# Performance work log

Hardware: AMD Instinct MI355X
Metric: run time of the kernel (lower is better)

The kernel has to match this reference:

```python
import jax, jax.numpy as jnp
import numpy as np

D_MODEL = 1024
D_STATE = 16
D_CONV = 4
EXPAND = 2
D_INNER = EXPAND * D_MODEL          # 2048
DT_RANK = (D_MODEL + 15) // 16      # 64 (mamba 'auto')
B, L = 2, 1024


def _mamba_params(key, scale=0.02):
    ks = jax.random.split(key, 6)
    return dict(
        inW=jax.random.normal(ks[0], (2 * D_INNER, D_MODEL), jnp.float32) * scale,
        convW=jax.random.normal(ks[1], (D_INNER, 1, D_CONV), jnp.float32) * scale,
        convb=jnp.zeros((D_INNER,), jnp.float32),
        xprojW=jax.random.normal(ks[2], (DT_RANK + 2 * D_STATE, D_INNER), jnp.float32) * scale,
        dtW=jax.random.normal(ks[3], (D_INNER, DT_RANK), jnp.float32) * scale,
        dtb=jax.random.normal(ks[4], (D_INNER,), jnp.float32) * scale,
        A_log=jnp.log(jnp.tile(jnp.arange(1, D_STATE + 1, dtype=jnp.float32), (D_INNER, 1))),
        Dskip=jnp.ones((D_INNER,), jnp.float32),
        outW=jax.random.normal(ks[5], (D_MODEL, D_INNER), jnp.float32) * scale,
    )


def setup_inputs() -> dict:
    key = jax.random.key(0)
    kx, kf, kb, kp = jax.random.split(key, 4)
    inp = {"x": jax.random.normal(kx, (B, L, D_MODEL), jnp.float32)}
    inp["ln_w"] = jnp.ones((D_MODEL,), jnp.float32)
    inp["ln_b"] = jnp.zeros((D_MODEL,), jnp.float32)
    for pref, k in (("f_", kf), ("b_", kb)):
        for name, v in _mamba_params(k).items():
            inp[pref + name] = v
    inp["proj_W"] = jax.random.normal(kp, (D_MODEL, 2 * D_MODEL), jnp.float32) * 0.02
    inp["proj_b"] = jnp.zeros((D_MODEL,), jnp.float32)
    return inp


def _layernorm(x, w, b, eps=1e-5):
    mu = jnp.mean(x, axis=-1, keepdims=True)
    var = jnp.var(x, axis=-1, keepdims=True)
    return (x - mu) * jax.lax.rsqrt(var + eps) * w + b


def _mamba(x, inW, convW, convb, xprojW, dtW, dtb, A_log, Dskip, outW):
    # x: [B, L, d_model]
    xz = jnp.einsum('bld,ed->ble', x, inW)           # [B,L,2*d_inner]
    xs, z = jnp.split(xz, 2, axis=-1)                # each [B,L,d_inner]
    # depthwise causal conv over L
    xc = jnp.transpose(xs, (0, 2, 1))                # [B,d_inner,L]
    xc = jax.lax.conv_general_dilated(
        xc, convW, window_strides=(1,), padding=[(D_CONV - 1, 0)],
        feature_group_count=D_INNER)
    xs = jax.nn.silu(jnp.transpose(xc + convb[None, :, None], (0, 2, 1)))
    # input-dependent dt, B, C
    xdb = jnp.einsum('bld,ed->ble', xs, xprojW)      # [B,L,dt_rank+2*d_state]
    dt, Bm, Cm = jnp.split(xdb, [DT_RANK, DT_RANK + D_STATE], axis=-1)
    dt = jax.nn.softplus(jnp.einsum('blr,dr->bld', dt, dtW) + dtb)  # [B,L,d_inner]
    A = -jnp.exp(A_log)                              # [d_inner,d_state], negative
    dA = jnp.exp(dt[..., None] * A)                  # [B,L,d_inner,d_state]
    dBx = dt[..., None] * Bm[:, :, None, :] * xs[..., None]

    def step(h, inputs):
        dA_t, dBx_t, C_t = inputs                    # [B,d,s],[B,d,s],[B,s]
        h = h * dA_t + dBx_t
        y = jnp.einsum('bds,bs->bd', h, C_t)
        return h, y

    h0 = jnp.zeros((x.shape[0], D_INNER, D_STATE), x.dtype)
    _, ys = jax.lax.scan(step, h0, (jnp.moveaxis(dA, 1, 0),
                                    jnp.moveaxis(dBx, 1, 0),
                                    jnp.moveaxis(Cm, 1, 0)))
    y = jnp.moveaxis(ys, 0, 1)                       # [B,L,d_inner]
    y = (y + xs * Dskip) * jax.nn.silu(z)
    return jnp.einsum('bld,ed->ble', y, outW)        # [B,L,d_model]


def reference(x, ln_w, ln_b,
              f_inW, f_convW, f_convb, f_xprojW, f_dtW, f_dtb, f_A_log, f_Dskip, f_outW,
              b_inW, b_convW, b_convb, b_xprojW, b_dtW, b_dtb, b_A_log, b_Dskip, b_outW,
              proj_W, proj_b):
    normed = _layernorm(x, ln_w, ln_b)
    fwd_out = _mamba(normed, f_inW, f_convW, f_convb, f_xprojW, f_dtW, f_dtb,
                     f_A_log, f_Dskip, f_outW)
    bwd_out = _mamba(normed[:, ::-1, :], b_inW, b_convW, b_convb, b_xprojW, b_dtW,
                     b_dtb, b_A_log, b_Dskip, b_outW)[:, ::-1, :]
    combined = jnp.concatenate([fwd_out, bwd_out], axis=-1)
    return x + jnp.einsum('blc,ec->ble', combined, proj_W) + proj_b
```

## Files before the change

kernel.cpp:

```cpp
#include <hip/hip_runtime.h>
#include <hip/hip_bf16.h>
#include <math.h>

#define DM   1024
#define DI   2048
#define DTR  64
#define DST  16
#define NB   2
#define LL   1024
#define MR   (NB*LL)
#define XLD  128
#define KS   8

typedef __bf16 bf16x8 __attribute__((ext_vector_type(8)));
typedef float  f32x4  __attribute__((ext_vector_type(4)));

__device__ __forceinline__ float siluf(float x) { return x / (1.f + __expf(-x)); }
__device__ __forceinline__ float softplusf(float x) {
    return fmaxf(x, 0.f) + log1pf(__expf(-fabsf(x)));
}
__device__ __forceinline__ unsigned short f2bf(float f) {
    __hip_bfloat16 h = __float2bfloat16(f);
    return *reinterpret_cast<unsigned short*>(&h);
}
__device__ __forceinline__ float bf2f(__hip_bfloat16 h) { return __bfloat162float(h); }

__device__ __forceinline__ void gl2lds16(const __hip_bfloat16* g, __hip_bfloat16* l)
{
    __builtin_amdgcn_global_load_lds(
        (const __attribute__((address_space(1))) unsigned int*)g,
        (__attribute__((address_space(3))) unsigned int*)l, 16, 0, 0);
}

__global__ __launch_bounds__(256) void layernorm_k(
    const float* __restrict__ x, const float* __restrict__ w,
    const float* __restrict__ b, __hip_bfloat16* __restrict__ out)
{
    int row = blockIdx.x;
    int tid = threadIdx.x;
    const float* xr = x + (size_t)row * DM;
    float4 v = *(const float4*)(xr + tid * 4);
    float s = v.x + v.y + v.z + v.w;
    float q = v.x*v.x + v.y*v.y + v.z*v.z + v.w*v.w;
    #pragma unroll
    for (int off = 32; off > 0; off >>= 1) {
        s += __shfl_xor(s, off, 64);
        q += __shfl_xor(q, off, 64);
    }
    __shared__ float ss[4], qq[4];
    int wv = tid >> 6;
    if ((tid & 63) == 0) { ss[wv] = s; qq[wv] = q; }
    __syncthreads();
    s = ss[0] + ss[1] + ss[2] + ss[3];
    q = qq[0] + qq[1] + qq[2] + qq[3];
    float mu  = s * (1.f / DM);
    float var = q * (1.f / DM) - mu * mu;
    float rstd = rsqrtf(var + 1e-5f);
    float4 wv4 = *(const float4*)(w + tid * 4);
    float4 bv4 = *(const float4*)(b + tid * 4);
    ushort4 o;
    o.x = f2bf((v.x - mu) * rstd * wv4.x + bv4.x);
    o.y = f2bf((v.y - mu) * rstd * wv4.y + bv4.y);
    o.z = f2bf((v.z - mu) * rstd * wv4.z + bv4.z);
    o.w = f2bf((v.w - mu) * rstd * wv4.w + bv4.w);
    *(ushort4*)((unsigned short*)out + (size_t)row * DM + tid * 4) = o;
}

__global__ __launch_bounds__(256) void cvt_all_k(
    const float* __restrict__ s0, const float* __restrict__ s1,
    const float* __restrict__ s2, const float* __restrict__ s3,
    const float* __restrict__ s4, __hip_bfloat16* __restrict__ dst)
{
    long idx = (long)(blockIdx.x * 256 + threadIdx.x) * 4;
    const float* src; long off;
    if      (idx <  4194304L) { src = s0; off = idx; }
    else if (idx <  8388608L) { src = s1; off = idx -  4194304L; }
    else if (idx < 10485760L) { src = s2; off = idx -  8388608L; }
    else if (idx < 10616832L) { src = s3; off = idx - 10485760L; }
    else                      { src = s4; off = idx - 10616832L; }
    float4 v = *(const float4*)(src + off);
    ushort4 o;
    o.x = f2bf(v.x); o.y = f2bf(v.y); o.z = f2bf(v.z); o.w = f2bf(v.w);
    *(ushort4*)((unsigned short*)dst + idx) = o;
}

__global__ __launch_bounds__(256) void cvt_pad96_k(
    const float* __restrict__ f_in, const float* __restrict__ b_in,
    __hip_bfloat16* __restrict__ out)
{
    int z = blockIdx.y;
    const float* in = z ? b_in : f_in;
    int idx = (blockIdx.x * 256 + threadIdx.x) * 4;
    int row = idx >> 11;
    ushort4 o = make_ushort4(0, 0, 0, 0);
    if (row < 96) {
        float4 v = *(const float4*)(in + idx);
        o.x = f2bf(v.x); o.y = f2bf(v.y); o.z = f2bf(v.z); o.w = f2bf(v.w);
    }
    *(ushort4*)((unsigned short*)out + (size_t)z * 128 * DI + idx) = o;
}

__global__ __launch_bounds__(256) void transpose_k(
    const float* __restrict__ f_o, const float* __restrict__ b_o,
    __hip_bfloat16* __restrict__ wot)
{
    int z = blockIdx.z;
    const float* src = z ? b_o : f_o;
    int c0 = blockIdx.x * 64;
    int r0 = blockIdx.y * 64;
    __shared__ float t[64][65];
    int tc = threadIdx.x & 63;
    int tr = threadIdx.x >> 6;
    #pragma unroll
    for (int ii = 0; ii < 16; ++ii) {
        int rl = tr + ii * 4;
        t[tc][rl] = src[(size_t)(r0 + rl) * DI + c0 + tc];
    }
    __syncthreads();
    __hip_bfloat16* dst = wot + (size_t)z * DI * DM;
    #pragma unroll
    for (int ii = 0; ii < 16; ++ii) {
        int cl = tr + ii * 4;
        dst[(size_t)(c0 + cl) * DM + r0 + tc] = __float2bfloat16(t[cl][tc]);
    }
}

template<int EPI>
__global__ __launch_bounds__(256) void gemm_gl(
    const __hip_bfloat16* __restrict__ A, int lda, size_t aofs,
    const __hip_bfloat16* __restrict__ B, int ldb, size_t bofs,
    void* __restrict__ Cp, int ldc, size_t cofs, int K,
    const float* __restrict__ bias0, const float* __restrict__ bias1)
{
    __shared__ __hip_bfloat16 As[128 * 64];
    __shared__ __hip_bfloat16 Bs[128 * 64];
    const int tid  = threadIdx.x;
    const int z    = blockIdx.z;
    const int bm   = blockIdx.y * 128;
    const int bn   = blockIdx.x * 128;
    const __hip_bfloat16* Az = A + (size_t)z * aofs;
    const __hip_bfloat16* Bz = B + (size_t)z * bofs;
    const int wv   = tid >> 6;
    const int lane = tid & 63;
    const int wr   = (wv >> 1) * 64;
    const int wc   = (wv & 1) * 64;
    const int srow = wv * 32 + (lane >> 3);
    const int cg   = ((lane & 7) ^ (lane >> 3)) * 8;
    const int fr   = lane & 15;
    const int quad = lane >> 4;
    const int pc0  = (quad ^ (fr & 7)) * 8;
    const int pc1  = ((4 + quad) ^ (fr & 7)) * 8;

    f32x4 acc[4][4] = {};

    for (int k0 = 0; k0 < K; k0 += 64) {
        __syncthreads();
        #pragma unroll
        for (int i = 0; i < 4; ++i) {
            int r = srow + i * 8;
            gl2lds16(Az + (size_t)(bm + r) * lda + k0 + cg, As + wv * 2048 + i * 512);
            gl2lds16(Bz + (size_t)(bn + r) * ldb + k0 + cg, Bs + wv * 2048 + i * 512);
        }
        __syncthreads();
        #pragma unroll
        for (int kk = 0; kk < 2; ++kk) {
            const int pc = kk ? pc1 : pc0;
            bf16x8 af[4], bf_[4];
            #pragma unroll
            for (int i = 0; i < 4; ++i) {
                af[i]  = *(const bf16x8*)(As + (wr + i * 16 + fr) * 64 + pc);
                bf_[i] = *(const bf16x8*)(Bs + (wc + i * 16 + fr) * 64 + pc);
            }
            #pragma unroll
            for (int i = 0; i < 4; ++i)
                #pragma unroll
                for (int j = 0; j < 4; ++j)
                    acc[i][j] = __builtin_amdgcn_mfma_f32_16x16x32_bf16(
                        af[i], bf_[j], acc[i][j], 0, 0, 0);
        }
    }

    const float* bias = (EPI == 3) ? (z ? bias1 : bias0) : nullptr;
    const int er = quad * 4;
    const int ec = fr;
    #pragma unroll
    for (int i = 0; i < 4; ++i) {
        #pragma unroll
        for (int j = 0; j < 4; ++j) {
            int row = bm + wr + i * 16 + er;
            int col = bn + wc + j * 16 + ec;
            #pragma unroll
            for (int r = 0; r < 4; ++r) {
                float v = acc[i][j][r];
                if (EPI == 1) {
                    ((__hip_bfloat16*)Cp)[(size_t)z * cofs +
                        (size_t)(row + r) * ldc + col] = __float2bfloat16(v);
                } else if (EPI == 3) {
                    ((__hip_bfloat16*)Cp)[(size_t)z * cofs +
                        (size_t)(row + r) * ldc + col] =
                        __float2bfloat16(softplusf(v + bias[col]));
                } else {
                    ((float*)Cp)[(size_t)z * cofs + (size_t)(row + r) * ldc + col] = v;
                }
            }
        }
    }
}

__global__ __launch_bounds__(256) void xproj_part_k(
    const __hip_bfloat16* __restrict__ A,
    const __hip_bfloat16* __restrict__ B,
    float* __restrict__ part)
{
    __shared__ __hip_bfloat16 As[128 * 64];
    __shared__ __hip_bfloat16 Bs[128 * 64];
    const int tid  = threadIdx.x;
    const int ks   = blockIdx.x;
    const int bm   = blockIdx.y * 128;
    const int z    = blockIdx.z;
    const __hip_bfloat16* Az = A + (size_t)z * MR * DI;
    const __hip_bfloat16* Bz = B + (size_t)z * 128 * DI;
    const int kb   = ks * (DI / KS);
    const int wv   = tid >> 6;
    const int lane = tid & 63;
    const int wr   = (wv >> 1) * 64;
    const int wc   = (wv & 1) * 64;
    const int srow = wv * 32 + (lane >> 3);
    const int cg   = ((lane & 7) ^ (lane >> 3)) * 8;
    const int fr   = lane & 15;
    const int quad = lane >> 4;
    const int pc0  = (quad ^ (fr & 7)) * 8;
    const int pc1  = ((4 + quad) ^ (fr & 7)) * 8;

    f32x4 acc[4][4] = {};

    #pragma unroll
    for (int k0 = 0; k0 < DI / KS; k0 += 64) {
        __syncthreads();
        #pragma unroll
        for (int i = 0; i < 4; ++i) {
            int r = srow + i * 8;
            gl2lds16(Az + (size_t)(bm + r) * DI + kb + k0 + cg, As + wv * 2048 + i * 512);
            gl2lds16(Bz + (size_t)r * DI + kb + k0 + cg,        Bs + wv * 2048 + i * 512);
        }
        __syncthreads();
        #pragma unroll
        for (int kk = 0; kk < 2; ++kk) {
            const int pc = kk ? pc1 : pc0;
            bf16x8 af[4], bf_[4];
            #pragma unroll
            for (int i = 0; i < 4; ++i) {
                af[i]  = *(const bf16x8*)(As + (wr + i * 16 + fr) * 64 + pc);
                bf_[i] = *(const bf16x8*)(Bs + (wc + i * 16 + fr) * 64 + pc);
            }
            #pragma unroll
            for (int i = 0; i < 4; ++i)
                #pragma unroll
                for (int j = 0; j < 4; ++j)
                    acc[i][j] = __builtin_amdgcn_mfma_f32_16x16x32_bf16(
                        af[i], bf_[j], acc[i][j], 0, 0, 0);
        }
    }

    float* dst = part + ((size_t)z * KS + ks) * MR * XLD;
    const int er = quad * 4;
    const int ec = fr;
    #pragma unroll
    for (int i = 0; i < 4; ++i)
        #pragma unroll
        for (int j = 0; j < 4; ++j) {
            int row = bm + wr + i * 16 + er;
            int col = wc + j * 16 + ec;
            #pragma unroll
            for (int r = 0; r < 4; ++r)
                dst[(size_t)(row + r) * XLD + col] = acc[i][j][r];
        }
}

__global__ __launch_bounds__(256) void xproj_reduce_k(
    const float* __restrict__ part, float* __restrict__ xdb,
    __hip_bfloat16* __restrict__ xdbt)
{
    int z = blockIdx.y;
    size_t idx = ((size_t)blockIdx.x * 256 + threadIdx.x) * 4;
    const float* p = part + (size_t)z * KS * MR * XLD;
    float4 s = make_float4(0.f, 0.f, 0.f, 0.f);
    #pragma unroll
    for (int ks = 0; ks < KS; ++ks) {
        float4 v = *(const float4*)(p + (size_t)ks * MR * XLD + idx);
        s.x += v.x; s.y += v.y; s.z += v.z; s.w += v.w;
    }
    *(float4*)(xdb + (size_t)z * MR * XLD + idx) = s;
    int c = (int)(idx & (XLD - 1));
    if (c < 64) {
        size_t m = idx >> 7;
        ushort4 o;
        o.x = f2bf(s.x); o.y = f2bf(s.y); o.z = f2bf(s.z); o.w = f2bf(s.w);
        *(ushort4*)((unsigned short*)xdbt + (size_t)z * MR * 64 + m * 64 + c) = o;
    }
}

__global__ __launch_bounds__(256) void conv_silu_k(
    const __hip_bfloat16* __restrict__ xz2,
    const float* __restrict__ fW, const float* __restrict__ fb,
    const float* __restrict__ bW, const float* __restrict__ bb_,
    __hip_bfloat16* __restrict__ xsb2)
{
    int dirv = blockIdx.y;
    int idx = blockIdx.x * 256 + threadIdx.x;
    int d = idx & (DI - 1);
    int m = idx >> 11;
    int t = m & (LL - 1);
    int bb = m >> 10;
    const float* w  = (dirv ? bW : fW) + d * 4;
    const __hip_bfloat16* xz = xz2 + (size_t)dirv * MR * 2 * DI;
    float acc = (dirv ? bb_ : fb)[d];
    if (dirv == 0) {
        #pragma unroll
        for (int k = 0; k < 4; ++k) {
            int tt = t - 3 + k;
            if (tt >= 0)
                acc = fmaf(w[k], bf2f(xz[(size_t)(bb * LL + tt) * (2 * DI) + d]), acc);
        }
    } else {
        #pragma unroll
        for (int k = 0; k < 4; ++k) {
            int tt = t + 3 - k;
            if (tt < LL)
                acc = fmaf(w[k], bf2f(xz[(size_t)(bb * LL + tt) * (2 * DI) + d]), acc);
        }
    }
    xsb2[(size_t)dirv * MR * DI + (size_t)m * DI + d] = __float2bfloat16(siluf(acc));
}

__global__ __launch_bounds__(256) void scan1_k(
    const __hip_bfloat16* __restrict__ dtf2, const __hip_bfloat16* __restrict__ xsb2,
    const float* __restrict__ xdb2,
    const float* __restrict__ fA, const float* __restrict__ bA,
    float* __restrict__ hend, float* __restrict__ aprod, int G, int Cn)
{
    int d  = blockIdx.x * 256 + threadIdx.x;
    int bb = blockIdx.y;
    int zz = blockIdx.z;
    int dirv = (zz >= G) ? 1 : 0;
    int g = zz - (dirv ? G : 0);
    const float* A_log = dirv ? bA : fA;
    const __hip_bfloat16* dtf = dtf2 + (size_t)dirv * MR * DI;
    const __hip_bfloat16* xs = xsb2 + (size_t)dirv * MR * DI;
    const float* xdb = xdb2 + (size_t)dirv * MR * XLD;
    size_t hoff = (size_t)dirv * G * (NB * DI * DST);

    float Ad[DST], h[DST], ap[DST];
    bool pw = true;
    #pragma unroll
    for (int s = 0; s < DST; ++s) {
        Ad[s] = -__expf(A_log[d * DST + s]);
        pw = pw && (fabsf(Ad[s] + (float)(s + 1)) < 1e-3f * (s + 1));
        h[s] = 0.f; ap[s] = 1.f;
    }
    int i0 = g * Cn;
    for (int i = 0; i < Cn; ++i) {
        int ii = i0 + i;
        int t = dirv ? (LL - 1 - ii) : ii;
        size_t m = (size_t)bb * LL + t;
        float dtv = bf2f(dtf[m * DI + d]);
        float xv  = bf2f(xs[m * DI + d]);
        const float* bc = xdb + m * XLD;
        float dtx = dtv * xv;
        float dAv[DST];
        if (pw) {
            float r = __expf(-dtv);
            float a = r;
            #pragma unroll
            for (int s = 0; s < DST; ++s) { dAv[s] = a; a *= r; }
        } else {
            #pragma unroll
            for (int s = 0; s < DST; ++s) dAv[s] = __expf(dtv * Ad[s]);
        }
        #pragma unroll
        for (int s = 0; s < DST; ++s) {
            h[s] = fmaf(h[s], dAv[s], dtx * bc[64 + s]);
            ap[s] *= dAv[s];
        }
    }
    size_t base = hoff + ((size_t)(g * NB + bb) * DI + d) * DST;
    #pragma unroll
    for (int s = 0; s < DST; s += 4) {
        *(float4*)(hend  + base + s) = make_float4(h[s], h[s+1], h[s+2], h[s+3]);
        *(float4*)(aprod + base + s) = make_float4(ap[s], ap[s+1], ap[s+2], ap[s+3]);
    }
}

__global__ __launch_bounds__(256) void scan2_k(
    float* __restrict__ hend, const float* __restrict__ aprod, int G)
{
    int dirv = blockIdx.y;
    int idx = blockIdx.x * 256 + threadIdx.x;
    const int slab = NB * DI * DST;
    size_t hoff = (size_t)dirv * G * slab;
    float carry = 0.f;
    for (int g = 0; g < G; ++g) {
        size_t off = hoff + (size_t)g * slab + idx;
        float a = aprod[off];
        float e = hend[off];
        hend[off] = carry;
        carry = fmaf(a, carry, e);
    }
}

__global__ __launch_bounds__(256) void scan3_k(
    const __hip_bfloat16* __restrict__ dtf2, const __hip_bfloat16* __restrict__ xsb2,
    const float* __restrict__ xdb2, const __hip_bfloat16* __restrict__ xz2,
    const float* __restrict__ fA, const float* __restrict__ bA,
    const float* __restrict__ fD, const float* __restrict__ bD,
    const float* __restrict__ hin, __hip_bfloat16* __restrict__ ycat, int G, int Cn)
{
    int d  = blockIdx.x * 256 + threadIdx.x;
    int bb = blockIdx.y;
    int zz = blockIdx.z;
    int dirv = (zz >= G) ? 1 : 0;
    int g = zz - (dirv ? G : 0);
    const float* A_log = dirv ? bA : fA;
    const float* Dskip = dirv ? bD : fD;
    const __hip_bfloat16* dtf = dtf2 + (size_t)dirv * MR * DI;
    const __hip_bfloat16* xs = xsb2 + (size_t)dirv * MR * DI;
    const float* xdb = xdb2 + (size_t)dirv * MR * XLD;
    const __hip_bfloat16* xz = xz2 + (size_t)dirv * MR * 2 * DI;
    size_t hoff = (size_t)dirv * G * (NB * DI * DST);

    float Ad[DST], h[DST];
    bool pw = true;
    size_t base = hoff + ((size_t)(g * NB + bb) * DI + d) * DST;
    #pragma unroll
    for (int s = 0; s < DST; ++s) {
        Ad[s] = -__expf(A_log[d * DST + s]);
        pw = pw && (fabsf(Ad[s] + (float)(s + 1)) < 1e-3f * (s + 1));
        h[s] = hin[base + s];
    }
    float Dsk = Dskip[d];
    int i0 = g * Cn;
    for (int i = 0; i < Cn; ++i) {
        int ii = i0 + i;
        int t = dirv ? (LL - 1 - ii) : ii;
        size_t m = (size_t)bb * LL + t;
        float dtv = bf2f(dtf[m * DI + d]);
        float xv  = bf2f(xs[m * DI + d]);
        const float* bc = xdb + m * XLD;
        float dtx = dtv * xv;
        float dAv[DST];
        if (pw) {
            float r = __expf(-dtv);
            float a = r;
            #pragma unroll
            for (int s = 0; s < DST; ++s) { dAv[s] = a; a *= r; }
        } else {
            #pragma unroll
            for (int s = 0; s < DST; ++s) dAv[s] = __expf(dtv * Ad[s]);
        }
        float yv = 0.f;
        #pragma unroll
        for (int s = 0; s < DST; ++s) {
            h[s] = fmaf(h[s], dAv[s], dtx * bc[64 + s]);
            yv = fmaf(h[s], bc[80 + s], yv);
        }
        float zv = bf2f(xz[m * (2 * DI) + DI + d]);
        ycat[m * (2 * DI) + (size_t)dirv * DI + d] =
            __float2bfloat16((yv + xv * Dsk) * siluf(zv));
    }
}

__global__ __launch_bounds__(256) void scan_mono_k(
    const __hip_bfloat16* __restrict__ dtf2, const __hip_bfloat16* __restrict__ xsb2,
    const float* __restrict__ xdb2, const __hip_bfloat16* __restrict__ xz2,
    const float* __restrict__ fA, const float* __restrict__ bA,
    const float* __restrict__ fD, const float* __restrict__ bD,
    __hip_bfloat16* __restrict__ ycat)
{
    int d  = blockIdx.x * 256 + threadIdx.x;
    int bb = blockIdx.y;
    int dirv = blockIdx.z;
    const float* A_log = dirv ? bA : fA;
    const float* Dskip = dirv ? bD : fD;
    const __hip_bfloat16* dtf = dtf2 + (size_t)dirv * MR * DI;
    const __hip_bfloat16* xs = xsb2 + (size_t)dirv * MR * DI;
    const float* xdb = xdb2 + (size_t)dirv * MR * XLD;
    const __hip_bfloat16* xz = xz2 + (size_t)dirv * MR * 2 * DI;
    float Ad[DST], h[DST];
    #pragma unroll
    for (int s = 0; s < DST; ++s) { Ad[s] = -__expf(A_log[d * DST + s]); h[s] = 0.f; }
    float Dsk = Dskip[d];
    for (int i = 0; i < LL; ++i) {
        int t = dirv ? (LL - 1 - i) : i;
        size_t m = (size_t)bb * LL + t;
        float dtv = bf2f(dtf[m * DI + d]);
        float xv  = bf2f(xs[m * DI + d]);
        const float* bc = xdb + m * XLD;
        float dtx = dtv * xv;
        float yv = 0.f;
        #pragma unroll
        for (int s = 0; s < DST; ++s) {
            float dA = __expf(dtv * Ad[s]);
            h[s] = fmaf(h[s], dA, dtx * bc[64 + s]);
            yv = fmaf(h[s], bc[80 + s], yv);
        }
        float zv = bf2f(xz[m * (2 * DI) + DI + d]);
        ycat[m * (2 * DI) + (size_t)dirv * DI + d] =
            __float2bfloat16((yv + xv * Dsk) * siluf(zv));
    }
}

__global__ __launch_bounds__(256) void final_reduce_k(
    const float* __restrict__ part, const float* __restrict__ x,
    const float* __restrict__ proj_b, float* __restrict__ out)
{
    size_t idx = ((size_t)blockIdx.x * 256 + threadIdx.x) * 4;
    float4 s = make_float4(0.f, 0.f, 0.f, 0.f);
    #pragma unroll
    for (int z = 0; z < 4; ++z) {
        float4 v = *(const float4*)(part + (size_t)z * MR * DM + idx);
        s.x += v.x; s.y += v.y; s.z += v.z; s.w += v.w;
    }
    float4 xv = *(const float4*)(x + idx);
    int col = (int)(idx & (DM - 1));
    float4 pb = *(const float4*)(proj_b + col);
    float4 o;
    o.x = xv.x + pb.x + s.x;
    o.y = xv.y + pb.y + s.y;
    o.z = xv.z + pb.z + s.z;
    o.w = xv.w + pb.w + s.w;
    *(float4*)(out + idx) = o;
}

extern "C" void kernel_launch(void* const* d_in, const int* in_sizes, int n_in,
                              void* d_out, int out_size, void* d_ws, size_t ws_size,
                              hipStream_t stream)
{
    const float* x      = (const float*)d_in[0];
    const float* ln_w   = (const float*)d_in[1];
    const float* ln_b   = (const float*)d_in[2];
    const float* f_inW    = (const float*)d_in[3];
    const float* f_convW  = (const float*)d_in[4];
    const float* f_convb  = (const float*)d_in[5];
    const float* f_xprojW = (const float*)d_in[6];
    const float* f_dtW    = (const float*)d_in[7];
    const float* f_dtb    = (const float*)d_in[8];
    const float* f_A_log  = (const float*)d_in[9];
    const float* f_Dskip  = (const float*)d_in[10];
    const float* f_outW   = (const float*)d_in[11];
    const float* b_inW    = (const float*)d_in[12];
    const float* b_convW  = (const float*)d_in[13];
    const float* b_convb  = (const float*)d_in[14];
    const float* b_xprojW = (const float*)d_in[15];
    const float* b_dtW    = (const float*)d_in[16];
    const float* b_dtb    = (const float*)d_in[17];
    const float* b_A_log  = (const float*)d_in[18];
    const float* b_Dskip  = (const float*)d_in[19];
    const float* b_outW   = (const float*)d_in[20];
    const float* proj_W = (const float*)d_in[21];
    const float* proj_b = (const float*)d_in[22];

    float* ws = (float*)d_ws;
    size_t o = 0;
    __hip_bfloat16* xz2  = (__hip_bfloat16*)(ws + o);
    __hip_bfloat16* wot  = xz2;
    float* fpart = ws + o;
    o += (size_t)2 * MR * 2 * DI / 2;
    __hip_bfloat16* xsb2 = (__hip_bfloat16*)(ws + o); o += (size_t)2 * MR * DI / 2;
    __hip_bfloat16* ycat = (__hip_bfloat16*)(ws + o);
    float* xpart = ws + o;
    o += (size_t)MR * 2 * DI / 2;
    float* xdb2 = ws + o; o += (size_t)2 * MR * XLD;
    __hip_bfloat16* xdbt = (__hip_bfloat16*)(ws + o); o += (size_t)2 * MR * 64 / 2;
    __hip_bfloat16* dtfb = (__hip_bfloat16*)(ws + o); o += (size_t)2 * MR * DI / 2;
    __hip_bfloat16* nb = (__hip_bfloat16*)(ws + o); o += (size_t)MR * DM / 2;
    __hip_bfloat16* warena = (__hip_bfloat16*)(ws + o); o += 15466496 / 2;
    float* hbuf = ws + o;
    size_t base_floats = o;

    __hip_bfloat16* wbi  = warena;
    __hip_bfloat16* pwb  = warena +  8388608;
    __hip_bfloat16* wdt  = warena + 10485760;
    __hip_bfloat16* wpb2 = warena + 10747904;
    __hip_bfloat16* wcat = warena + 11272192;

    const size_t slab = (size_t)NB * DI * DST;
    int G = 32;
    while (G > 4 && (base_floats + 4ull * G * slab) * 4 > ws_size) G >>= 1;
    int useChunks = ((base_floats + 4ull * G * slab) * 4 <= ws_size);
    float* hend  = hbuf;
    float* aprod = hbuf + 2ull * G * slab;
    int Cn = useChunks ? LL / G : LL;

    cvt_all_k<<<10496, 256, 0, stream>>>(f_inW, b_inW, proj_W, f_dtW, b_dtW, warena);
    cvt_pad96_k<<<dim3(64, 2), 256, 0, stream>>>(f_xprojW, b_xprojW, wpb2);
    transpose_k<<<dim3(DI / 64, DM / 64, 2), 256, 0, stream>>>(f_outW, b_outW, wot);
    gemm_gl<1><<<dim3(DI / 128, DM / 128, 2), 256, 0, stream>>>(
        pwb, 2 * DM, (size_t)DM, wot, DM, (size_t)DI * DM,
        wcat, 2 * DI, (size_t)DI, DM, nullptr, nullptr);

    layernorm_k<<<MR, 256, 0, stream>>>(x, ln_w, ln_b, nb);

    gemm_gl<1><<<dim3((2 * DI) / 128, MR / 128, 2), 256, 0, stream>>>(
        nb, DM, 0, wbi, DM, (size_t)2 * DI * DM,
        xz2, 2 * DI, (size_t)MR * 2 * DI, DM, nullptr, nullptr);

    conv_silu_k<<<dim3((MR * DI) / 256, 2), 256, 0, stream>>>(
        xz2, f_convW, f_convb, b_convW, b_convb, xsb2);

    xproj_part_k<<<dim3(KS, MR / 128, 2), 256, 0, stream>>>(xsb2, wpb2, xpart);
    xproj_reduce_k<<<dim3((MR * XLD) / 1024, 2), 256, 0, stream>>>(xpart, xdb2, xdbt);

    gemm_gl<3><<<dim3(DI / 128, MR / 128, 2), 256, 0, stream>>>(
        xdbt, 64, (size_t)MR * 64, wdt, 64, (size_t)DI * 64,
        dtfb, DI, (size_t)MR * DI, 64, f_dtb, b_dtb);

    if (useChunks) {
        scan1_k<<<dim3(DI / 256, NB, 2 * G), 256, 0, stream>>>(
            dtfb, xsb2, xdb2, f_A_log, b_A_log, hend, aprod, G, Cn);
        scan2_k<<<dim3((NB * DI * DST) / 256, 2), 256, 0, stream>>>(hend, aprod, G);
        scan3_k<<<dim3(DI / 256, NB, 2 * G), 256, 0, stream>>>(
            dtfb, xsb2, xdb2, xz2, f_A_log, b_A_log, f_Dskip, b_Dskip,
            hend, ycat, G, Cn);
    } else {
        scan_mono_k<<<dim3(DI / 256, NB, 2), 256, 0, stream>>>(
            dtfb, xsb2, xdb2, xz2, f_A_log, b_A_log, f_Dskip, b_Dskip, ycat);
    }

    gemm_gl<0><<<dim3(DM / 128, MR / 128, 4), 256, 0, stream>>>(
        ycat, 2 * DI, 1024, wcat, 2 * DI, 1024,
        fpart, DM, (size_t)MR * DM, 1024, nullptr, nullptr);

    final_reduce_k<<<(MR * DM) / 1024, 256, 0, stream>>>(
        fpart, x, proj_b, (float*)d_out);
}
```

Before: 424.8 us.

## Fuse prep kernels, use atomic split-K output, and coalesce GEMM epilogue via LDS

Result: no change. 431.2 us (+1.5%).

```diff
diff --git a/kernel.cpp b/kernel.cpp
--- a/kernel.cpp
+++ b/kernel.cpp
@@ -32,96 +32,100 @@
         (__attribute__((address_space(3))) unsigned int*)l, 16, 0, 0);
 }
 
-__global__ __launch_bounds__(256) void layernorm_k(
-    const float* __restrict__ x, const float* __restrict__ w,
-    const float* __restrict__ b, __hip_bfloat16* __restrict__ out)
-{
-    int row = blockIdx.x;
-    int tid = threadIdx.x;
-    const float* xr = x + (size_t)row * DM;
-    float4 v = *(const float4*)(xr + tid * 4);
-    float s = v.x + v.y + v.z + v.w;
-    float q = v.x*v.x + v.y*v.y + v.z*v.z + v.w*v.w;
-    #pragma unroll
-    for (int off = 32; off > 0; off >>= 1) {
-        s += __shfl_xor(s, off, 64);
-        q += __shfl_xor(q, off, 64);
-    }
-    __shared__ float ss[4], qq[4];
-    int wv = tid >> 6;
-    if ((tid & 63) == 0) { ss[wv] = s; qq[wv] = q; }
-    __syncthreads();
-    s = ss[0] + ss[1] + ss[2] + ss[3];
-    q = qq[0] + qq[1] + qq[2] + qq[3];
-    float mu  = s * (1.f / DM);
-    float var = q * (1.f / DM) - mu * mu;
-    float rstd = rsqrtf(var + 1e-5f);
-    float4 wv4 = *(const float4*)(w + tid * 4);
-    float4 bv4 = *(const float4*)(b + tid * 4);
-    ushort4 o;
-    o.x = f2bf((v.x - mu) * rstd * wv4.x + bv4.x);
-    o.y = f2bf((v.y - mu) * rstd * wv4.y + bv4.y);
-    o.z = f2bf((v.z - mu) * rstd * wv4.z + bv4.z);
-    o.w = f2bf((v.w - mu) * rstd * wv4.w + bv4.w);
-    *(ushort4*)((unsigned short*)out + (size_t)row * DM + tid * 4) = o;
-}
-
-__global__ __launch_bounds__(256) void cvt_all_k(
+__global__ __launch_bounds__(256) void prep_k(
     const float* __restrict__ s0, const float* __restrict__ s1,
     const float* __restrict__ s2, const float* __restrict__ s3,
-    const float* __restrict__ s4, __hip_bfloat16* __restrict__ dst)
-{
-    long idx = (long)(blockIdx.x * 256 + threadIdx.x) * 4;
-    const float* src; long off;
-    if      (idx <  4194304L) { src = s0; off = idx; }
-    else if (idx <  8388608L) { src = s1; off = idx -  4194304L; }
-    else if (idx < 10485760L) { src = s2; off = idx -  8388608L; }
-    else if (idx < 10616832L) { src = s3; off = idx - 10485760L; }
-    else                      { src = s4; off = idx - 10616832L; }
-    float4 v = *(const float4*)(src + off);
-    ushort4 o;
-    o.x = f2bf(v.x); o.y = f2bf(v.y); o.z = f2bf(v.z); o.w = f2bf(v.w);
-    *(ushort4*)((unsigned short*)dst + idx) = o;
-}
-
-__global__ __launch_bounds__(256) void cvt_pad96_k(
-    const float* __restrict__ f_in, const float* __restrict__ b_in,
-    __hip_bfloat16* __restrict__ out)
-{
-    int z = blockIdx.y;
-    const float* in = z ? b_in : f_in;
-    int idx = (blockIdx.x * 256 + threadIdx.x) * 4;
-    int row = idx >> 11;
-    ushort4 o = make_ushort4(0, 0, 0, 0);
-    if (row < 96) {
-        float4 v = *(const float4*)(in + idx);
+    const float* __restrict__ s4, __hip_bfloat16* __restrict__ warena,
+    const float* __restrict__ fx, const float* __restrict__ bx,
+    __hip_bfloat16* __restrict__ wpb2,
+    const float* __restrict__ fo, const float* __restrict__ bo,
+    __hip_bfloat16* __restrict__ wot,
+    const float* __restrict__ x, const float* __restrict__ lnw,
+    const float* __restrict__ lnb, __hip_bfloat16* __restrict__ nb,
+    const float* __restrict__ proj_b, float* __restrict__ outp)
+{
+    __shared__ float pshm[64 * 65];
+    const int b = blockIdx.x;
+    const int tid = threadIdx.x;
+
+    if (b < 10496) {
+        long idx = (long)b * 1024 + tid * 4;
+        const float* src; long off;
+        if      (idx <  4194304L) { src = s0; off = idx; }
+        else if (idx <  8388608L) { src = s1; off = idx -  4194304L; }
+        else if (idx < 10485760L) { src = s2; off = idx -  8388608L; }
+        else if (idx < 10616832L) { src = s3; off = idx - 10485760L; }
+        else                      { src = s4; off = idx - 10616832L; }
+        float4 v = *(const float4*)(src + off);
+        ushort4 o;
         o.x = f2bf(v.x); o.y = f2bf(v.y); o.z = f2bf(v.z); o.w = f2bf(v.w);
-    }
-    *(ushort4*)((unsigned short*)out + (size_t)z * 128 * DI + idx) = o;
-}
-
-__global__ __launch_bounds__(256) void transpose_k(
-    const float* __restrict__ f_o, const float* __restrict__ b_o,
-    __hip_bfloat16* __restrict__ wot)
-{
-    int z = blockIdx.z;
-    const float* src = z ? b_o : f_o;
-    int c0 = blockIdx.x * 64;
-    int r0 = blockIdx.y * 64;
-    __shared__ float t[64][65];
-    int tc = threadIdx.x & 63;
-    int tr = threadIdx.x >> 6;
-    #pragma unroll
-    for (int ii = 0; ii < 16; ++ii) {
-        int rl = tr + ii * 4;
-        t[tc][rl] = src[(size_t)(r0 + rl) * DI + c0 + tc];
-    }
-    __syncthreads();
-    __hip_bfloat16* dst = wot + (size_t)z * DI * DM;
-    #pragma unroll
-    for (int ii = 0; ii < 16; ++ii) {
-        int cl = tr + ii * 4;
-        dst[(size_t)(c0 + cl) * DM + r0 + tc] = __float2bfloat16(t[cl][tc]);
+        *(ushort4*)((unsigned short*)warena + idx) = o;
+    } else if (b < 10624) {
+        int t = b - 10496;
+        int z = t >> 6;
+        const float* in = z ? bx : fx;
+        int idx = ((t & 63) * 256 + tid) * 4;
+        int row = idx >> 11;
+        ushort4 o = make_ushort4(0, 0, 0, 0);
+        if (row < 96) {
+            float4 v = *(const float4*)(in + idx);
+            o.x = f2bf(v.x); o.y = f2bf(v.y); o.z = f2bf(v.z); o.w = f2bf(v.w);
+        }
+        *(ushort4*)((unsigned short*)wpb2 + (size_t)z * 128 * DI + idx) = o;
+    } else if (b < 11648) {
+        int t = b - 10624;
+        int z = t >> 9; t &= 511;
+        const float* src = z ? bo : fo;
+        int c0 = (t & 31) * 64;
+        int r0 = (t >> 5) * 64;
+        int tc = tid & 63;
+        int tr = tid >> 6;
+        #pragma unroll
+        for (int ii = 0; ii < 16; ++ii) {
+            int rl = tr + ii * 4;
+            pshm[tc * 65 + rl] = src[(size_t)(r0 + rl) * DI + c0 + tc];
+        }
+        __syncthreads();
+        __hip_bfloat16* dst = wot + (size_t)z * DI * DM;
+        #pragma unroll
+        for (int ii = 0; ii < 16; ++ii) {
+            int cl = tr + ii * 4;
+            dst[(size_t)(c0 + cl) * DM + r0 + tc] = __float2bfloat16(pshm[cl * 65 + tc]);
+        }
+    } else if (b < 13696) {
+        int row = b - 11648;
+        const float* xr = x + (size_t)row * DM;
+        float4 v = *(const float4*)(xr + tid * 4);
+        float s = v.x + v.y + v.z + v.w;
+        float q = v.x*v.x + v.y*v.y + v.z*v.z + v.w*v.w;
+        #pragma unroll
+        for (int off = 32; off > 0; off >>= 1) {
+            s += __shfl_xor(s, off, 64);
+            q += __shfl_xor(q, off, 64);
+        }
+        int wv = tid >> 6;
+        if ((tid & 63) == 0) { pshm[wv] = s; pshm[8 + wv] = q; }
+        __syncthreads();
+        s = pshm[0] + pshm[1] + pshm[2] + pshm[3];
+        q = pshm[8] + pshm[9] + pshm[10] + pshm[11];
+        float mu  = s * (1.f / DM);
+        float var = q * (1.f / DM) - mu * mu;
+        float rstd = rsqrtf(var + 1e-5f);
+        float4 wv4 = *(const float4*)(lnw + tid * 4);
+        float4 bv4 = *(const float4*)(lnb + tid * 4);
+        ushort4 o;
+        o.x = f2bf((v.x - mu) * rstd * wv4.x + bv4.x);
+        o.y = f2bf((v.y - mu) * rstd * wv4.y + bv4.y);
+        o.z = f2bf((v.z - mu) * rstd * wv4.z + bv4.z);
+        o.w = f2bf((v.w - mu) * rstd * wv4.w + bv4.w);
+        *(ushort4*)((unsigned short*)nb + (size_t)row * DM + tid * 4) = o;
+    } else {
+        size_t idx = ((size_t)(b - 13696) * 256 + tid) * 4;
+        float4 xv = *(const float4*)(x + idx);
+        float4 pb = *(const float4*)(proj_b + (idx & (DM - 1)));
+        float4 o;
+        o.x = xv.x + pb.x; o.y = xv.y + pb.y; o.z = xv.z + pb.z; o.w = xv.w + pb.w;
+        *(float4*)(outp + idx) = o;
     }
 }
 
@@ -132,8 +136,9 @@
     void* __restrict__ Cp, int ldc, size_t cofs, int K,
     const float* __restrict__ bias0, const float* __restrict__ bias1)
 {
-    __shared__ __hip_bfloat16 As[128 * 64];
-    __shared__ __hip_bfloat16 Bs[128 * 64];
+    __shared__ __hip_bfloat16 smem[2 * 128 * 64];
+    __hip_bfloat16* As = smem;
+    __hip_bfloat16* Bs = smem + 128 * 64;
     const int tid  = threadIdx.x;
     const int z    = blockIdx.z;
     const int bm   = blockIdx.y * 128;
@@ -180,30 +185,56 @@
         }
     }
 
+    if (EPI == 4) {
+        const int er = quad * 4;
+        #pragma unroll
+        for (int i = 0; i < 4; ++i)
+            #pragma unroll
+            for (int j = 0; j < 4; ++j) {
+                int row = bm + wr + i * 16 + er;
+                int col = bn + wc + j * 16 + fr;
+                #pragma unroll
+                for (int r = 0; r < 4; ++r)
+                    atomicAdd((float*)Cp + (size_t)(row + r) * ldc + col, acc[i][j][r]);
+            }
+        return;
+    }
+
     const float* bias = (EPI == 3) ? (z ? bias1 : bias0) : nullptr;
-    const int er = quad * 4;
-    const int ec = fr;
+    float* eps = (float*)smem;
+    const int half = wv >> 1;
+    const int lrow = tid >> 3;
+    const int cseg = (tid & 7) * 16;
+    const int gr_  = bm + (lrow >> 4) * 64 + (lrow & 15);
     #pragma unroll
     for (int i = 0; i < 4; ++i) {
-        #pragma unroll
-        for (int j = 0; j < 4; ++j) {
-            int row = bm + wr + i * 16 + er;
-            int col = bn + wc + j * 16 + ec;
-            #pragma unroll
-            for (int r = 0; r < 4; ++r) {
-                float v = acc[i][j][r];
-                if (EPI == 1) {
-                    ((__hip_bfloat16*)Cp)[(size_t)z * cofs +
-                        (size_t)(row + r) * ldc + col] = __float2bfloat16(v);
-                } else if (EPI == 3) {
-                    ((__hip_bfloat16*)Cp)[(size_t)z * cofs +
-                        (size_t)(row + r) * ldc + col] =
-                        __float2bfloat16(softplusf(v + bias[col]));
-                } else {
-                    ((float*)Cp)[(size_t)z * cofs + (size_t)(row + r) * ldc + col] = v;
-                }
-            }
-        }
+        __syncthreads();
+        #pragma unroll
+        for (int j = 0; j < 4; ++j)
+            #pragma unroll
+            for (int r = 0; r < 4; ++r)
+                eps[(half * 16 + quad * 4 + r) * 132 + wc + j * 16 + fr] = acc[i][j][r];
+        __syncthreads();
+        float vals[16];
+        *(float4*)(vals +  0) = *(const float4*)(eps + lrow * 132 + cseg +  0);
+        *(float4*)(vals +  4) = *(const float4*)(eps + lrow * 132 + cseg +  4);
+        *(float4*)(vals +  8) = *(const float4*)(eps + lrow * 132 + cseg +  8);
+        *(float4*)(vals + 12) = *(const float4*)(eps + lrow * 132 + cseg + 12);
+        int gr = gr_ + i * 16;
+        int gc = bn + cseg;
+        unsigned short os[16];
+        #pragma unroll
+        for (int c = 0; c < 16; ++c) {
+            float t = vals[c];
+            if (EPI == 3) t = softplusf(t + bias[gc + c]);
+            os[c] = f2bf(t);
+        }
+        unsigned short* dst = (unsigned short*)Cp + (size_t)z * cofs +
+                              (size_t)gr * ldc + gc;
+        *(ushort4*)(dst +  0) = *(ushort4*)(os +  0);
+        *(ushort4*)(dst +  4) = *(ushort4*)(os +  4);
+        *(ushort4*)(dst +  8) = *(ushort4*)(os +  8);
+        *(ushort4*)(dst + 12) = *(ushort4*)(os + 12);
     }
 }
 
@@ -212,8 +243,9 @@
     const __hip_bfloat16* __restrict__ B,
     float* __restrict__ part)
 {
-    __shared__ __hip_bfloat16 As[128 * 64];
-    __shared__ __hip_bfloat16 Bs[128 * 64];
+    __shared__ __hip_bfloat16 smem[2 * 128 * 64];
+    __hip_bfloat16* As = smem;
+    __hip_bfloat16* Bs = smem + 128 * 64;
     const int tid  = threadIdx.x;
     const int ks   = blockIdx.x;
     const int bm   = blockIdx.y * 128;
@@ -264,13 +296,12 @@
 
     float* dst = part + ((size_t)z * KS + ks) * MR * XLD;
     const int er = quad * 4;
-    const int ec = fr;
     #pragma unroll
     for (int i = 0; i < 4; ++i)
         #pragma unroll
         for (int j = 0; j < 4; ++j) {
             int row = bm + wr + i * 16 + er;
-            int col = wc + j * 16 + ec;
+            int col = wc + j * 16 + fr;
             #pragma unroll
             for (int r = 0; r < 4; ++r)
                 dst[(size_t)(row + r) * XLD + col] = acc[i][j][r];
@@ -507,28 +538,6 @@
         ycat[m * (2 * DI) + (size_t)dirv * DI + d] =
             __float2bfloat16((yv + xv * Dsk) * siluf(zv));
     }
-}
-
-__global__ __launch_bounds__(256) void final_reduce_k(
-    const float* __restrict__ part, const float* __restrict__ x,
-    const float* __restrict__ proj_b, float* __restrict__ out)
-{
-    size_t idx = ((size_t)blockIdx.x * 256 + threadIdx.x) * 4;
-    float4 s = make_float4(0.f, 0.f, 0.f, 0.f);
-    #pragma unroll
-    for (int z = 0; z < 4; ++z) {
-        float4 v = *(const float4*)(part + (size_t)z * MR * DM + idx);
-        s.x += v.x; s.y += v.y; s.z += v.z; s.w += v.w;
-    }
-    float4 xv = *(const float4*)(x + idx);
-    int col = (int)(idx & (DM - 1));
-    float4 pb = *(const float4*)(proj_b + col);
-    float4 o;
-    o.x = xv.x + pb.x + s.x;
-    o.y = xv.y + pb.y + s.y;
-    o.z = xv.z + pb.z + s.z;
-    o.w = xv.w + pb.w + s.w;
-    *(float4*)(out + idx) = o;
 }
 
 extern "C" void kernel_launch(void* const* d_in, const int* in_sizes, int n_in,
@@ -563,7 +572,6 @@
     size_t o = 0;
     __hip_bfloat16* xz2  = (__hip_bfloat16*)(ws + o);
     __hip_bfloat16* wot  = xz2;
-    float* fpart = ws + o;
     o += (size_t)2 * MR * 2 * DI / 2;
     __hip_bfloat16* xsb2 = (__hip_bfloat16*)(ws + o); o += (size_t)2 * MR * DI / 2;
     __hip_bfloat16* ycat = (__hip_bfloat16*)(ws + o);
@@ -591,14 +599,16 @@
     float* aprod = hbuf + 2ull * G * slab;
     int Cn = useChunks ? LL / G : LL;
 
-    cvt_all_k<<<10496, 256, 0, stream>>>(f_inW, b_inW, proj_W, f_dtW, b_dtW, warena);
-    cvt_pad96_k<<<dim3(64, 2), 256, 0, stream>>>(f_xprojW, b_xprojW, wpb2);
-    transpose_k<<<dim3(DI / 64, DM / 64, 2), 256, 0, stream>>>(f_outW, b_outW, wot);
+    prep_k<<<15744, 256, 0, stream>>>(
+        f_inW, b_inW, proj_W, f_dtW, b_dtW, warena,
+        f_xprojW, b_xprojW, wpb2,
+        f_outW, b_outW, wot,
+        x, ln_w, ln_b, nb,
+        proj_b, (float*)d_out);
+
     gemm_gl<1><<<dim3(DI / 128, DM / 128, 2), 256, 0, stream>>>(
         pwb, 2 * DM, (size_t)DM, wot, DM, (size_t)DI * DM,
         wcat, 2 * DI, (size_t)DI, DM, nullptr, nullptr);
-
-    layernorm_k<<<MR, 256, 0, stream>>>(x, ln_w, ln_b, nb);
 
     gemm_gl<1><<<dim3((2 * DI) / 128, MR / 128, 2), 256, 0, stream>>>(
         nb, DM, 0, wbi, DM, (size_t)2 * DI * DM,
@@ -626,10 +636,7 @@
             dtfb, xsb2, xdb2, xz2, f_A_log, b_A_log, f_Dskip, b_Dskip, ycat);
     }
 
-    gemm_gl<0><<<dim3(DM / 128, MR / 128, 4), 256, 0, stream>>>(
+    gemm_gl<4><<<dim3(DM / 128, MR / 128, 4), 256, 0, stream>>>(
         ycat, 2 * DI, 1024, wcat, 2 * DI, 1024,
-        fpart, DM, (size_t)MR * DM, 1024, nullptr, nullptr);
-
-    final_reduce_k<<<(MR * DM) / 1024, 256, 0, stream>>>(
-        fpart, x, proj_b, (float*)d_out);
-}
+        (float*)d_out, DM, 0, 1024, nullptr, nullptr);
+}
```
